# Optimization experiments

Measured on AMD Instinct MI355X. Metric: run time of the kernel, lower is better.

## Reference

```python
import jax, jax.numpy as jnp
import numpy as np

L = 128          # lifted_dim
NS = 50000       # source nodes
NT = 50000       # target nodes
E = 640000       # edges
SLOPE = 0.01     # cfg.leaky_slope (torch LeakyReLU default)
EPS = 1e-5       # BatchNorm eps


def _glorot(key, shape):
    fan_in, fan_out = shape[0], shape[1]
    lim = np.sqrt(6.0 / (fan_in + fan_out)).astype(np.float32)
    return jax.random.uniform(key, shape, jnp.float32, -lim, lim)


def setup_inputs() -> dict:
    key = jax.random.key(0)
    ks = jax.random.split(key, 16)
    x_s = jax.random.normal(ks[0], (NS, L), jnp.float32)
    x_t = jax.random.normal(ks[1], (NT, L), jnp.float32)
    edge_index = jax.random.randint(ks[2], (2, E), 0, NT, jnp.int64)
    edge_attr = jax.random.normal(ks[3], (E, L), jnp.float32)
    x_u = jax.random.normal(ks[4], (L,), jnp.float32)
    M = 2 * L  # message_dim
    U = 4 * L  # update_dim
    params = {
        'W1': _glorot(ks[5], (M, M)), 'b1': jnp.zeros((M,), jnp.float32),
        'W2': _glorot(ks[6], (M, M)), 'b2': jnp.zeros((M,), jnp.float32),
        'U1': _glorot(ks[7], (U, U)), 'c1': jnp.zeros((U,), jnp.float32),
        'U2': _glorot(ks[8], (U, L)), 'c2': jnp.zeros((L,), jnp.float32),
        'gamma': jnp.ones((L,), jnp.float32), 'beta': jnp.zeros((L,), jnp.float32),
    }
    return dict(x_s=x_s, x_t=x_t, edge_index=edge_index, edge_attr=edge_attr, x_u=x_u, **params)


def reference(x_s, x_t, edge_index, edge_attr, x_u,
              W1, b1, W2, b2, U1, c1, U2, c2, gamma, beta):
    src, tgt = edge_index[0], edge_index[1]
    # edge messages: gather source features + edge attrs -> 2-layer MLP
    msg = jnp.concatenate([x_s[src], edge_attr], axis=1)          # [E, 2L]
    msg = jax.nn.leaky_relu(msg @ W1 + b1, negative_slope=SLOPE)
    msg = msg @ W2 + b2                                           # [E, 2L]
    # scatter-add aggregation onto target nodes
    agg = jax.ops.segment_sum(msg, tgt, num_segments=x_t.shape[0])  # [NT, 2L]
    # node update
    xu = jnp.broadcast_to(x_u[None, :], (x_t.shape[0], x_u.shape[0]))
    h = jnp.concatenate([x_t, agg, xu], axis=-1)                  # [NT, 4L]
    h = jax.nn.leaky_relu(h @ U1 + c1, negative_slope=SLOPE)
    h = h @ U2 + c2                                               # [NT, L]
    # BatchNorm1d (training mode: batch statistics, biased variance)
    mu = jnp.mean(h, axis=0)
    var = jnp.var(h, axis=0)
    return gamma * (h - mu) * jax.lax.rsqrt(var + EPS) + beta
```

## Files before the change

kernel.cpp:

```cpp
#include <hip/hip_runtime.h>

typedef unsigned int u32;
typedef unsigned short u16;
typedef __attribute__((ext_vector_type(8))) short short8;
typedef __attribute__((ext_vector_type(8))) unsigned short ushort8v;
typedef __attribute__((ext_vector_type(4))) unsigned short ushort4v;
typedef __attribute__((ext_vector_type(4))) float f32x4;

#define NSRC 50000
#define NTGT 50000
#define NEDGE 640000
#define LDIM 128
#define SLOPE 0.01f

#define MFMA(a, b, c) __builtin_amdgcn_mfma_f32_16x16x32_bf16((a), (b), (c), 0, 0, 0)

__device__ __forceinline__ u16 f2bf(float f) {
  union { float f; u32 u; } v; v.f = f;
  u32 r = v.u + 0x7FFFu + ((v.u >> 16) & 1u);
  return (u16)(r >> 16);
}
__device__ __forceinline__ float bf2f(u16 h) {
  union { u32 u; float f; } v; v.u = ((u32)h) << 16; return v.f;
}

__global__ void k_w2b(const float* __restrict__ W2, const float* __restrict__ U1,
                      float* __restrict__ w2b) {
  const int i = blockIdx.x;
  const int j = threadIdx.x;
  const float* __restrict__ u = U1 + (size_t)128 * 512;
  float a0 = 0.f, a1 = 0.f;
#pragma unroll 8
  for (int k = 0; k < 256; ++k) {
    float w = W2[(size_t)i * 256 + k];
    a0 += w * u[(size_t)k * 512 + j];
    a1 += w * u[(size_t)k * 512 + j + 256];
  }
  w2b[(size_t)i * 512 + j] = a0;
  w2b[(size_t)i * 512 + j + 256] = a1;
}

__global__ void k_bias(const float* __restrict__ U1, const float* __restrict__ xu,
                       const float* __restrict__ b2, const float* __restrict__ c1,
                       float* __restrict__ c1e, float* __restrict__ vb) {
  const int j = threadIdx.x;
  float s = c1[j];
#pragma unroll 4
  for (int k = 0; k < 128; ++k) s += xu[k] * U1[(size_t)(384 + k) * 512 + j];
  float v = 0.f;
#pragma unroll 4
  for (int k = 0; k < 256; ++k) v += b2[k] * U1[(size_t)(128 + k) * 512 + j];
  c1e[j] = s;
  vb[j] = v;
}

__global__ void k_prep(const float* __restrict__ W1, const float* __restrict__ U1,
                       const float* __restrict__ U2, const float* __restrict__ w2b,
                       u16* __restrict__ w1a, u16* __restrict__ w1b,
                       u16* __restrict__ u1e, u16* __restrict__ u2p) {
  int id = blockIdx.x * 256 + threadIdx.x;
  int lane = id & 63, quad = (lane >> 4), l16 = lane & 15;
  if (id < 4096) {
    int g = id >> 6;
    int kc = g >> 4, cb = g & 15;
    const float* s = W1 + (size_t)(kc * 32 + quad * 8) * 256 + cb * 16 + l16;
    ushort8v p;
#pragma unroll
    for (int j = 0; j < 8; ++j) p[j] = f2bf(s[(size_t)j * 256]);
    *(ushort8v*)(w1a + ((size_t)g * 64 + lane) * 8) = p;
  } else if (id < 8192) {
    int g = (id - 4096) >> 6;
    int kc = g >> 4, cb = g & 15;
    const float* s = W1 + (size_t)(128 + kc * 32 + quad * 8) * 256 + cb * 16 + l16;
    ushort8v p;
#pragma unroll
    for (int j = 0; j < 8; ++j) p[j] = f2bf(s[(size_t)j * 256]);
    *(ushort8v*)(w1b + ((size_t)g * 64 + lane) * 8) = p;
  } else if (id < 32768) {
    int g = (id - 8192) >> 6;
    int kc = g >> 5, cb = g & 31;
    int col = cb * 16 + l16;
    ushort8v p;
#pragma unroll
    for (int j = 0; j < 8; ++j) {
      int row = kc * 32 + quad * 8 + j;
      float v = (row < 128) ? U1[(size_t)row * 512 + col]
                            : w2b[(size_t)(row - 128) * 512 + col];
      p[j] = f2bf(v);
    }
    *(ushort8v*)(u1e + ((size_t)g * 64 + lane) * 8) = p;
  } else if (id < 40960) {
    int g = (id - 32768) >> 6;
    int kc = g >> 3, cb = g & 7;
    const float* s = U2 + (size_t)(kc * 32 + quad * 8) * 128 + cb * 16 + l16;
    ushort8v p;
#pragma unroll
    for (int j = 0; j < 8; ++j) p[j] = f2bf(s[(size_t)j * 128]);
    *(ushort8v*)(u2p + ((size_t)g * 64 + lane) * 8) = p;
  }
}

__global__ void k_count(const int* __restrict__ tgt, int* __restrict__ cnt,
                        int* __restrict__ rank) {
  int e = blockIdx.x * 256 + threadIdx.x;
  if (e < NEDGE) rank[e] = atomicAdd(&cnt[tgt[e]], 1);
}

__global__ void k_scan(const int* __restrict__ cnt, int* __restrict__ rowstart) {
  __shared__ int part[1024];
  int tid = threadIdx.x;
  int base = tid * 49;
  int s = 0;
  for (int i = 0; i < 49; ++i) { int idx = base + i; if (idx < NTGT) s += cnt[idx]; }
  part[tid] = s;
  __syncthreads();
  for (int off = 1; off < 1024; off <<= 1) {
    int v = (tid >= off) ? part[tid - off] : 0;
    __syncthreads();
    part[tid] += v;
    __syncthreads();
  }
  int run = (tid > 0) ? part[tid - 1] : 0;
  for (int i = 0; i < 49; ++i) {
    int idx = base + i;
    if (idx < NTGT) { rowstart[idx] = run; run += cnt[idx]; }
  }
  if (tid == 1023) rowstart[NTGT] = part[1023];
}

__global__ void k_posinv(const int* __restrict__ tgt, const int* __restrict__ rowstart,
                         const int* __restrict__ rank, int* __restrict__ order) {
  int e = blockIdx.x * 256 + threadIdx.x;
  if (e < NEDGE) order[rowstart[tgt[e]] + rank[e]] = e;
}

__global__ __launch_bounds__(256, 3) void k_pgemm(
    const float* __restrict__ xs, const u16* __restrict__ w1ap,
    const float* __restrict__ b1, u16* __restrict__ P) {
  __shared__ u16 At[64][136];
  __shared__ u16 Ot[64][264];
  const int tid = threadIdx.x;
  const int base = blockIdx.x * 64;
  {
    const int et = tid >> 2, p = tid & 3;
    const int row = base + et;
    u16* dst = &At[et][p * 32];
    if (row < NSRC) {
      const float4* f4 = (const float4*)(xs + (size_t)row * LDIM + p * 32);
#pragma unroll
      for (int i = 0; i < 4; ++i) {
        float4 a = f4[2 * i], b = f4[2 * i + 1];
        ushort8v pk = { f2bf(a.x), f2bf(a.y), f2bf(a.z), f2bf(a.w),
                        f2bf(b.x), f2bf(b.y), f2bf(b.z), f2bf(b.w) };
        *(ushort8v*)(dst + i * 8) = pk;
      }
    } else {
      ushort8v z = {0, 0, 0, 0, 0, 0, 0, 0};
#pragma unroll
      for (int i = 0; i < 4; ++i) *(ushort8v*)(dst + i * 8) = z;
    }
  }
  __syncthreads();

  const int lane = tid & 63, wid = tid >> 6;
  const int quad = lane >> 4, l16 = lane & 15;
  const int colb = wid * 64;
  const short8* __restrict__ wf = (const short8*)w1ap;

  f32x4 acc[4][4];
#pragma unroll
  for (int a = 0; a < 4; ++a)
#pragma unroll
    for (int b = 0; b < 4; ++b) acc[a][b] = (f32x4){0.f, 0.f, 0.f, 0.f};
#pragma unroll
  for (int kc = 0; kc < 4; ++kc) {
    short8 af[4], bfr[4];
#pragma unroll
    for (int ct = 0; ct < 4; ++ct)
      bfr[ct] = wf[(size_t)(kc * 16 + wid * 4 + ct) * 64 + lane];
#pragma unroll
    for (int rt = 0; rt < 4; ++rt)
      af[rt] = *(const short8*)&At[rt * 16 + l16][kc * 32 + quad * 8];
#pragma unroll
    for (int rt = 0; rt < 4; ++rt)
#pragma unroll
      for (int ct = 0; ct < 4; ++ct)
        acc[rt][ct] = MFMA(af[rt], bfr[ct], acc[rt][ct]);
  }
#pragma unroll
  for (int ct = 0; ct < 4; ++ct) {
    int col = colb + ct * 16 + l16;
    float bias = b1[col];
#pragma unroll
    for (int rt = 0; rt < 4; ++rt)
#pragma unroll
      for (int r = 0; r < 4; ++r) {
        int row = rt * 16 + quad * 4 + r;
        Ot[row][col] = f2bf(acc[rt][ct][r] + bias);
      }
  }
  __syncthreads();
  {
    const int et = tid >> 2, p = tid & 3;
    const int row = base + et;
    if (row < NSRC) {
      u16* dst = P + (size_t)row * 256 + p * 64;
      const u16* sl = &Ot[et][p * 64];
#pragma unroll
      for (int i = 0; i < 8; ++i)
        *(ushort8v*)(dst + i * 8) = *(const ushort8v*)(sl + i * 8);
    }
  }
}

__global__ __launch_bounds__(256, 4) void k_edge(
    const float* __restrict__ ea, const int* __restrict__ srcp,
    const int* __restrict__ tgtp, const int* __restrict__ order,
    const u16* __restrict__ Pg, const u16* __restrict__ w1bp,
    float* __restrict__ agg) {
  __shared__ u16 Pt[64][264];
  __shared__ int s_tgt[64];
  __shared__ unsigned long long s_mask;
  const int tid = threadIdx.x;
  const int base = blockIdx.x * 64;

  {
    const int et = tid >> 2, p = tid & 3;
    const int e = order[base + et];
    if (p == 0) s_tgt[et] = tgtp[e];
    const int sidx = srcp[e];
    const ushort8v* pr = (const ushort8v*)(Pg + (size_t)sidx * 256 + p * 64);
    u16* dst = &Pt[et][p * 64];
#pragma unroll
    for (int i = 0; i < 8; ++i) *(ushort8v*)(dst + i * 8) = pr[i];
  }
  if (tid < 64) {
    int tcur = tgtp[order[base + tid]];
    int tprv = (tid > 0) ? tgtp[order[base + tid - 1]] : tcur;
    unsigned long long m = __ballot(tcur != tprv);
    if (tid == 0) s_mask = m;
  }

  const int lane = tid & 63, wid = tid >> 6;
  const int quad = lane >> 4, l16 = lane & 15;
  const int colb = wid * 64;
  const short8* __restrict__ wf = (const short8*)w1bp;

  const float* ab[4];
#pragma unroll
  for (int rt = 0; rt < 4; ++rt)
    ab[rt] = ea + (size_t)order[base + rt * 16 + l16] * LDIM + quad * 8;

  f32x4 acc[4][4];
#pragma unroll
  for (int a = 0; a < 4; ++a)
#pragma unroll
    for (int b = 0; b < 4; ++b) acc[a][b] = (f32x4){0.f, 0.f, 0.f, 0.f};

#pragma unroll
  for (int kc = 0; kc < 4; ++kc) {
    short8 af[4];
#pragma unroll
    for (int rt = 0; rt < 4; ++rt) {
      f32x4 x = *(const f32x4*)(ab[rt] + kc * 32);
      f32x4 y = *(const f32x4*)(ab[rt] + kc * 32 + 4);
      af[rt] = (short8){ (short)f2bf(x[0]), (short)f2bf(x[1]),
                         (short)f2bf(x[2]), (short)f2bf(x[3]),
                         (short)f2bf(y[0]), (short)f2bf(y[1]),
                         (short)f2bf(y[2]), (short)f2bf(y[3]) };
    }
    short8 bfr[4];
#pragma unroll
    for (int ct = 0; ct < 4; ++ct)
      bfr[ct] = wf[(size_t)(kc * 16 + wid * 4 + ct) * 64 + lane];
#pragma unroll
    for (int rt = 0; rt < 4; ++rt)
#pragma unroll
      for (int ct = 0; ct < 4; ++ct)
        acc[rt][ct] = MFMA(af[rt], bfr[ct], acc[rt][ct]);
  }
  __syncthreads();

#pragma unroll
  for (int ct = 0; ct < 4; ++ct) {
    int col = colb + ct * 16 + l16;
#pragma unroll
    for (int rt = 0; rt < 4; ++rt)
#pragma unroll
      for (int r = 0; r < 4; ++r) {
        int row = rt * 16 + quad * 4 + r;
        float v = acc[rt][ct][r] + bf2f(Pt[row][col]);
        v = v > 0.f ? v : SLOPE * v;
        Pt[row][col] = f2bf(v);
      }
  }
  __syncthreads();

  {
    const unsigned long long mask = s_mask;
    const int col = tid;
    float accv = 0.f;
    int segstart = 0;
    for (int r = 0; r < 64; ++r) {
      if ((mask >> r) & 1ull) {
        float* dst = agg + (size_t)s_tgt[r - 1] * 256 + col;
        if (segstart == 0) atomicAdd(dst, accv);
        else *dst = accv;
        accv = 0.f; segstart = r;
      }
      accv += bf2f(Pt[r][col]);
    }
    atomicAdd(agg + (size_t)s_tgt[63] * 256 + col, accv);
  }
}

__global__ __launch_bounds__(256, 4) void k_node(
    const float* __restrict__ xt, const float* __restrict__ agg,
    const int* __restrict__ rowstart, const u16* __restrict__ u1e,
    const u16* __restrict__ u2p, const float* __restrict__ c1e,
    const float* __restrict__ vb, const float* __restrict__ c2,
    float* __restrict__ h2, float* __restrict__ stats) {
  __shared__ u16 ain[32][520];
  __shared__ float sdeg[32];
  const int tid = threadIdx.x;
  const int lane = tid & 63, wid = tid >> 6;
  const int quad = lane >> 4, l16 = lane & 15;
  const int tbase = blockIdx.x * 32;

  for (int s = wid; s < 32; s += 4) {
    int t = tbase + s;
    if (t < NTGT) {
      if (lane < 32) {
        float4 v = ((const float4*)(xt + (size_t)t * LDIM))[lane];
        ushort4v p = { f2bf(v.x), f2bf(v.y), f2bf(v.z), f2bf(v.w) };
        *(ushort4v*)&ain[s][lane * 4] = p;
      }
      if (lane == 0) sdeg[s] = (float)(rowstart[t + 1] - rowstart[t]);
      float4 v = ((const float4*)(agg + (size_t)t * 256))[lane];
      ushort4v p = { f2bf(v.x), f2bf(v.y), f2bf(v.z), f2bf(v.w) };
      *(ushort4v*)&ain[s][128 + lane * 4] = p;
    } else {
      ushort8v z = {0, 0, 0, 0, 0, 0, 0, 0};
      *(ushort8v*)&ain[s][lane * 8] = z;
      if (lane == 0) sdeg[s] = 0.f;
    }
  }
  __syncthreads();

  const short8* __restrict__ u1f = (const short8*)u1e;
  const short8* __restrict__ u2f = (const short8*)u2p;

  f32x4 acc[2][2][4];
#pragma unroll
  for (int h = 0; h < 2; ++h)
#pragma unroll
    for (int a = 0; a < 2; ++a)
#pragma unroll
      for (int b = 0; b < 4; ++b) acc[h][a][b] = (f32x4){0.f, 0.f, 0.f, 0.f};

#pragma unroll 2
  for (int kc = 0; kc < 12; ++kc) {
    short8 af[2];
#pragma unroll
    for (int rt = 0; rt < 2; ++rt)
      af[rt] = *(const short8*)&ain[rt * 16 + l16][kc * 32 + quad * 8];
#pragma unroll
    for (int h = 0; h < 2; ++h) {
      short8 bfr[4];
#pragma unroll
      for (int ct = 0; ct < 4; ++ct)
        bfr[ct] = u1f[(size_t)(kc * 32 + h * 16 + wid * 4 + ct) * 64 + lane];
#pragma unroll
      for (int rt = 0; rt < 2; ++rt)
#pragma unroll
        for (int ct = 0; ct < 4; ++ct)
          acc[h][rt][ct] = MFMA(af[rt], bfr[ct], acc[h][rt][ct]);
    }
  }
  __syncthreads();
#pragma unroll
  for (int h = 0; h < 2; ++h)
#pragma unroll
    for (int ct = 0; ct < 4; ++ct) {
      int col = h * 256 + wid * 64 + ct * 16 + l16;
      float cb = c1e[col], vbb = vb[col];
#pragma unroll
      for (int rt = 0; rt < 2; ++rt)
#pragma unroll
        for (int r = 0; r < 4; ++r) {
          int row = rt * 16 + quad * 4 + r;
          float v = acc[h][rt][ct][r] + cb + sdeg[row] * vbb;
          v = v > 0.f ? v : SLOPE * v;
          ain[row][col] = f2bf(v);
        }
    }
  __syncthreads();

  const int colb2 = wid * 32;
  f32x4 acc2[2][2];
#pragma unroll
  for (int a = 0; a < 2; ++a)
#pragma unroll
    for (int b = 0; b < 2; ++b) acc2[a][b] = (f32x4){0.f, 0.f, 0.f, 0.f};
#pragma unroll 4
  for (int kc = 0; kc < 16; ++kc) {
    short8 af[2], bfr[2];
#pragma unroll
    for (int ct = 0; ct < 2; ++ct)
      bfr[ct] = u2f[(size_t)(kc * 8 + wid * 2 + ct) * 64 + lane];
#pragma unroll
    for (int rt = 0; rt < 2; ++rt)
      af[rt] = *(const short8*)&ain[rt * 16 + l16][kc * 32 + quad * 8];
#pragma unroll
    for (int rt = 0; rt < 2; ++rt)
#pragma unroll
      for (int ct = 0; ct < 2; ++ct)
        acc2[rt][ct] = MFMA(af[rt], bfr[ct], acc2[rt][ct]);
  }
  float s1[2] = {0.f, 0.f}, s2[2] = {0.f, 0.f};
#pragma unroll
  for (int ct = 0; ct < 2; ++ct) {
    int col = colb2 + ct * 16 + l16;
    float cb = c2[col];
#pragma unroll
    for (int rt = 0; rt < 2; ++rt)
#pragma unroll
      for (int r = 0; r < 4; ++r) {
        int row = rt * 16 + quad * 4 + r;
        int t = tbase + row;
        if (t < NTGT) {
          float v = acc2[rt][ct][r] + cb;
          h2[(size_t)t * LDIM + col] = v;
          s1[ct] += v; s2[ct] += v * v;
        }
      }
  }
#pragma unroll
  for (int ct = 0; ct < 2; ++ct) {
    float a = s1[ct], b = s2[ct];
    a += __shfl_down(a, 32); b += __shfl_down(b, 32);
    a += __shfl_down(a, 16); b += __shfl_down(b, 16);
    if (lane < 16) {
      atomicAdd(&stats[colb2 + ct * 16 + l16], a);
      atomicAdd(&stats[128 + colb2 + ct * 16 + l16], b);
    }
  }
}

__global__ void k_bnfin(const float* __restrict__ stats, const float* __restrict__ gamma,
                        const float* __restrict__ beta, float* __restrict__ ss) {
  int c = threadIdx.x;
  if (c < 128) {
    float mu = stats[c] * (1.0f / NTGT);
    float var = stats[128 + c] * (1.0f / NTGT) - mu * mu;
    float rs = rsqrtf(var + 1e-5f);
    float sc = gamma[c] * rs;
    ss[c] = sc;
    ss[128 + c] = beta[c] - mu * sc;
  }
}

__global__ void k_bnapply(const float* __restrict__ h2, const float* __restrict__ ss,
                          float* __restrict__ out) {
  int i = blockIdx.x * 256 + threadIdx.x;
  const int total = NTGT * LDIM / 4;
  const float4* h4 = (const float4*)h2;
  const float4* sc4 = (const float4*)ss;
  const float4* sh4 = (const float4*)(ss + 128);
  float4* o4 = (float4*)out;
  for (; i < total; i += gridDim.x * 256) {
    int cg = i & 31;
    float4 h = h4[i], sc = sc4[cg], sh = sh4[cg];
    float4 r = { h.x * sc.x + sh.x, h.y * sc.y + sh.y,
                 h.z * sc.z + sh.z, h.w * sc.w + sh.w };
    o4[i] = r;
  }
}

extern "C" void kernel_launch(void* const* d_in, const int* in_sizes, int n_in,
                              void* d_out, int out_size, void* d_ws, size_t ws_size,
                              hipStream_t stream) {
  (void)in_sizes; (void)n_in; (void)out_size; (void)ws_size;
  const float* xs    = (const float*)d_in[0];
  const float* xt    = (const float*)d_in[1];
  const int*   ei    = (const int*)d_in[2];
  const float* ea    = (const float*)d_in[3];
  const float* xu    = (const float*)d_in[4];
  const float* W1    = (const float*)d_in[5];
  const float* b1    = (const float*)d_in[6];
  const float* W2    = (const float*)d_in[7];
  const float* b2    = (const float*)d_in[8];
  const float* U1    = (const float*)d_in[9];
  const float* c1    = (const float*)d_in[10];
  const float* U2    = (const float*)d_in[11];
  const float* c2    = (const float*)d_in[12];
  const float* gamma = (const float*)d_in[13];
  const float* beta  = (const float*)d_in[14];

  char* ws = (char*)d_ws;
  u16* w1a   = (u16*)(ws + 0x000000);
  u16* w1b   = (u16*)(ws + 0x010000);
  u16* u1e   = (u16*)(ws + 0x020000);
  u16* u2p   = (u16*)(ws + 0x080000);
  float* w2b = (float*)(ws + 0x0A0000);
  float* c1e = (float*)(ws + 0x120000);
  float* vbv = (float*)(ws + 0x120800);
  int* cnt   = (int*)(ws + 0x130000);
  int* rowst = (int*)(ws + 0x161000);
  int* rank  = (int*)(ws + 0x192000);
  float* stats = (float*)(ws + 0x404000);
  float* ss    = stats + 256;
  int* order = (int*)(ws + 0x405000);
  float* agg = (float*)(ws + 0x680000);
  u16*   Pbuf = (u16*)(ws + 0x3760000);
  float* h2   = (float*)(ws + 0x3760000);

  const int* srcp = ei;
  const int* tgtp = ei + NEDGE;

  hipMemsetAsync(cnt, 0, NTGT * 4, stream);
  hipMemsetAsync(stats, 0, 256 * 4, stream);
  hipMemsetAsync(agg, 0, (size_t)NTGT * 256 * 4, stream);
  k_w2b<<<256, 256, 0, stream>>>(W2, U1, w2b);
  k_bias<<<1, 512, 0, stream>>>(U1, xu, b2, c1, c1e, vbv);
  k_prep<<<160, 256, 0, stream>>>(W1, U1, U2, w2b, w1a, w1b, u1e, u2p);
  k_count<<<2500, 256, 0, stream>>>(tgtp, cnt, rank);
  k_scan<<<1, 1024, 0, stream>>>(cnt, rowst);
  k_posinv<<<2500, 256, 0, stream>>>(tgtp, rowst, rank, order);
  k_pgemm<<<782, 256, 0, stream>>>(xs, w1a, b1, Pbuf);
  k_edge<<<10000, 256, 0, stream>>>(ea, srcp, tgtp, order, Pbuf, w1b, agg);
  k_node<<<1563, 256, 0, stream>>>(xt, agg, rowst, u1e, u2p, c1e, vbv, c2, h2, stats);
  k_bnfin<<<1, 128, 0, stream>>>(stats, gamma, beta, ss);
  k_bnapply<<<6250, 256, 0, stream>>>(h2, ss, (float*)d_out);
}
```

Baseline: 984.9 us.

## Repartition edge GEMM so each wave owns 16 rows and all columns

Each wave in the edge-message kernel used to compute a 64x64 block, so every wave loaded and converted all 64 edge_attr rows. Now each wave computes 16 rows across all 256 output columns, in two halves of 128 columns. Each wave converts only its own row of fp32 edge attributes to bf16 once and keeps it in registers, which cuts redundant global loads and conversions by 4x. In exchange, every wave must now read all of the W1 B-fragments rather than a quarter of them, and the MFMA work is split into two sequential passes.

```diff
diff --git a/kernel.cpp b/kernel.cpp
--- a/kernel.cpp
+++ b/kernel.cpp
@@ -243,56 +243,63 @@
 
   const int lane = tid & 63, wid = tid >> 6;
   const int quad = lane >> 4, l16 = lane & 15;
-  const int colb = wid * 64;
   const short8* __restrict__ wf = (const short8*)w1bp;
 
-  const float* ab[4];
-#pragma unroll
-  for (int rt = 0; rt < 4; ++rt)
-    ab[rt] = ea + (size_t)order[base + rt * 16 + l16] * LDIM + quad * 8;
-
-  f32x4 acc[4][4];
-#pragma unroll
-  for (int a = 0; a < 4; ++a)
-#pragma unroll
-    for (int b = 0; b < 4; ++b) acc[a][b] = (f32x4){0.f, 0.f, 0.f, 0.f};
-
+  const int myrow = wid * 16 + l16;
+  const float* arow = ea + (size_t)order[base + myrow] * LDIM + quad * 8;
+
+  short8 af[4];
 #pragma unroll
   for (int kc = 0; kc < 4; ++kc) {
-    short8 af[4];
-#pragma unroll
-    for (int rt = 0; rt < 4; ++rt) {
-      f32x4 x = *(const f32x4*)(ab[rt] + kc * 32);
-      f32x4 y = *(const f32x4*)(ab[rt] + kc * 32 + 4);
-      af[rt] = (short8){ (short)f2bf(x[0]), (short)f2bf(x[1]),
-                         (short)f2bf(x[2]), (short)f2bf(x[3]),
-                         (short)f2bf(y[0]), (short)f2bf(y[1]),
-                         (short)f2bf(y[2]), (short)f2bf(y[3]) };
-    }
-    short8 bfr[4];
-#pragma unroll
-    for (int ct = 0; ct < 4; ++ct)
-      bfr[ct] = wf[(size_t)(kc * 16 + wid * 4 + ct) * 64 + lane];
-#pragma unroll
-    for (int rt = 0; rt < 4; ++rt)
-#pragma unroll
-      for (int ct = 0; ct < 4; ++ct)
-        acc[rt][ct] = MFMA(af[rt], bfr[ct], acc[rt][ct]);
-  }
-  __syncthreads();
-
-#pragma unroll
-  for (int ct = 0; ct < 4; ++ct) {
-    int col = colb + ct * 16 + l16;
-#pragma unroll
-    for (int rt = 0; rt < 4; ++rt)
-#pragma unroll
-      for (int r = 0; r < 4; ++r) {
-        int row = rt * 16 + quad * 4 + r;
-        float v = acc[rt][ct][r] + bf2f(Pt[row][col]);
-        v = v > 0.f ? v : SLOPE * v;
-        Pt[row][col] = f2bf(v);
-      }
+    f32x4 x = *(const f32x4*)(arow + kc * 32);
+    f32x4 y = *(const f32x4*)(arow + kc * 32 + 4);
+    af[kc] = (short8){ (short)f2bf(x[0]), (short)f2bf(x[1]),
+                       (short)f2bf(x[2]), (short)f2bf(x[3]),
+                       (short)f2bf(y[0]), (short)f2bf(y[1]),
+                       (short)f2bf(y[2]), (short)f2bf(y[3]) };
+  }
+
+  f32x4 acc[8];
+#pragma unroll
+  for (int ct = 0; ct < 8; ++ct) acc[ct] = (f32x4){0.f, 0.f, 0.f, 0.f};
+#pragma unroll
+  for (int kc = 0; kc < 4; ++kc)
+#pragma unroll
+    for (int ct = 0; ct < 8; ++ct)
+      acc[ct] = MFMA(af[kc], wf[(size_t)(kc * 16 + ct) * 64 + lane], acc[ct]);
+
+  __syncthreads();
+
+#pragma unroll
+  for (int ct = 0; ct < 8; ++ct) {
+    int col = ct * 16 + l16;
+#pragma unroll
+    for (int r = 0; r < 4; ++r) {
+      int row = wid * 16 + quad * 4 + r;
+      float v = acc[ct][r] + bf2f(Pt[row][col]);
+      v = v > 0.f ? v : SLOPE * v;
+      Pt[row][col] = f2bf(v);
+    }
+  }
+
+#pragma unroll
+  for (int ct = 0; ct < 8; ++ct) acc[ct] = (f32x4){0.f, 0.f, 0.f, 0.f};
+#pragma unroll
+  for (int kc = 0; kc < 4; ++kc)
+#pragma unroll
+    for (int ct = 0; ct < 8; ++ct)
+      acc[ct] = MFMA(af[kc], wf[(size_t)(kc * 16 + 8 + ct) * 64 + lane], acc[ct]);
+
+#pragma unroll
+  for (int ct = 0; ct < 8; ++ct) {
+    int col = 128 + ct * 16 + l16;
+#pragma unroll
+    for (int r = 0; r < 4; ++r) {
+      int row = wid * 16 + quad * 4 + r;
+      float v = acc[ct][r] + bf2f(Pt[row][col]);
+      v = v > 0.f ? v : SLOPE * v;
+      Pt[row][col] = f2bf(v);
+    }
   }
   __syncthreads();
 
```

New measurement: 948.6 us. 1.04x faster.
